# Kernel optimization log

Hardware: AMD Instinct MI355X
Metric: run time of the kernel (lower is better)

## Reference

```python
import jax, jax.numpy as jnp
import numpy as np

B, S, D, F, E = 8, 2048, 768, 3072, 8


def setup_inputs() -> dict:
    key = jax.random.key(0)
    k1, k2, k3, k4 = jax.random.split(key, 4)
    return {
        "hidden_states": jax.random.normal(k1, (B, S, D), dtype=jnp.float32),
        "router_w": jax.random.normal(k2, (D, E), dtype=jnp.float32) * 0.02,
        "w_in": jax.random.normal(k3, (E, D, F), dtype=jnp.float32) * 0.02,
        "w_out": jax.random.normal(k4, (E, F, D), dtype=jnp.float32) * 0.02,
    }


def reference(hidden_states, router_w, w_in, w_out):
    b, s, d = hidden_states.shape
    x = hidden_states.reshape(-1, d)                    # [T, D] tokens
    router_logits = x @ router_w                        # [T, E]
    router_probs_full = jax.nn.softmax(router_logits, axis=-1)
    expert_index = jnp.argmax(router_probs_full, axis=-1)          # top-1 routing
    onehot = jax.nn.one_hot(expert_index, E, dtype=x.dtype)        # [T, E] router_mask
    top_prob = jnp.max(router_probs_full, axis=-1, keepdims=True)  # [T, 1] router_probs

    # Per-expert FFN (relu MLP); every token is processed by exactly one expert,
    # expert outputs overwrite the token (gather/scatter combine in the original).
    y = jnp.zeros_like(x)
    for e in range(E):  # fixed small expert count; weights structurally distinct
        h = jax.nn.relu(x @ w_in[e]) @ w_out[e]
        y = y + onehot[:, e:e + 1] * h

    out = (top_prob * y).reshape(b, s, d)
    return out, router_logits, expert_index
```

## Files before the change

kernel.cpp:

```cpp
#include <hip/hip_runtime.h>
#include <hip/hip_bf16.h>

constexpr int T  = 16384;
constexpr int Dh = 768;
constexpr int Fh = 3072;
constexpr int Eh = 8;
constexpr int MAXT2 = T / 256 + Eh;

typedef unsigned short ushort_t;
typedef __attribute__((ext_vector_type(8))) short  bf16x8;
typedef __attribute__((ext_vector_type(4))) float  f32x4;

static __device__ __forceinline__ ushort_t f2bf(float f) {
    unsigned u = __builtin_bit_cast(unsigned, f);
    u += 0x7FFFu + ((u >> 16) & 1u);
    return (ushort_t)(u >> 16);
}

__global__ __launch_bounds__(1024) void router_kernel(
    const float* __restrict__ x, const float* __restrict__ rw,
    float* __restrict__ logits_out, float* __restrict__ eidx_out,
    float* __restrict__ topp, int* __restrict__ counts, int* __restrict__ perm) {

    __shared__ float rwT[Eh][Dh];
    __shared__ int   sAmax[16];
    __shared__ int   sBase[Eh];

    int tid = threadIdx.x;
    for (int i = tid; i < Dh * Eh; i += 1024) {
        int d = i >> 3, e = i & 7;
        rwT[e][d] = rw[i];
    }
    __syncthreads();

    int wave = tid >> 6, lane = tid & 63;
    int t = blockIdx.x * 16 + wave;
    const float* xr = x + (size_t)t * Dh;

    double acc[Eh];
#pragma unroll
    for (int e = 0; e < Eh; ++e) acc[e] = 0.0;

#pragma unroll
    for (int j = 0; j < Dh / 256; ++j) {
        int d = lane * 4 + j * 256;
        const float4 xv = *(const float4*)(xr + d);
#pragma unroll
        for (int e = 0; e < Eh; ++e) {
            const float4 w = *(const float4*)&rwT[e][d];
            acc[e] += (double)xv.x * (double)w.x + (double)xv.y * (double)w.y
                    + (double)xv.z * (double)w.z + (double)xv.w * (double)w.w;
        }
    }
#pragma unroll
    for (int off = 32; off > 0; off >>= 1) {
#pragma unroll
        for (int e = 0; e < Eh; ++e) acc[e] += __shfl_xor(acc[e], off, 64);
    }

    int amax = 0;
    if (lane == 0) {
        float l32[Eh];
        float m = -3.4e38f;
#pragma unroll
        for (int e = 0; e < Eh; ++e) l32[e] = (float)acc[e];
#pragma unroll
        for (int e = 0; e < Eh; ++e) {
            if (l32[e] > m) { m = l32[e]; amax = e; }
        }
        float s = 0.f;
#pragma unroll
        for (int e = 0; e < Eh; ++e) s += expf(l32[e] - m);
#pragma unroll
        for (int e = 0; e < Eh; ++e) logits_out[(size_t)t * Eh + e] = l32[e];
        eidx_out[t] = (float)amax;
        topp[t]     = 1.0f / s;
        sAmax[wave] = amax;
    }
    __syncthreads();

    if (tid < Eh) {
        int c = 0;
#pragma unroll
        for (int w = 0; w < 16; ++w) c += (sAmax[w] == tid);
        sBase[tid] = (c > 0) ? atomicAdd(&counts[tid], c) : 0;
    }
    __syncthreads();

    if (lane == 0) {
        int prior = 0;
        for (int w = 0; w < wave; ++w) prior += (sAmax[w] == amax);
        perm[amax * T + sBase[amax] + prior] = t;
    }
}

__global__ void scan_counts(const int* counts, int* offsets,
                            int* tE, int* tGoff, int* tSlot0, int* tRows, int* nT) {
    int lane = threadIdx.x;
    if (lane < Eh) {
        int coff = 0, toff = 0;
        for (int e = 0; e < lane; ++e) {
            int ce = counts[e];
            coff += ce;
            toff += (ce + 255) >> 8;
        }
        int c = counts[lane];
        offsets[lane] = coff;
        int myt = (c + 255) >> 8;
        for (int k = 0; k < myt; ++k) {
            int idx = toff + k;
            tE[idx]     = lane;
            tGoff[idx]  = coff + k * 256;
            tSlot0[idx] = k * 256;
            int rem = c - k * 256;
            tRows[idx]  = rem < 256 ? rem : 256;
        }
        if (lane == Eh - 1) {
            offsets[Eh] = coff + c;
            nT[0] = toff + myt;
        }
    }
}

__global__ void gather_cast_x(const float* __restrict__ x, const int* __restrict__ offsets,
                              const int* __restrict__ perm, ushort_t* __restrict__ Xg) {
    __shared__ int soff[Eh + 1];
    if (threadIdx.x < Eh + 1) soff[threadIdx.x] = offsets[threadIdx.x];
    __syncthreads();
    int q  = blockIdx.x * 256 + threadIdx.x;
    int g  = q / (Dh / 4);
    int cq = (q - g * (Dh / 4)) * 4;
    int e = 0;
#pragma unroll
    for (int i = 1; i < Eh; ++i) e += (g >= soff[i]);
    int tok = perm[e * T + (g - soff[e])];
    const float4 v = *(const float4*)(x + (size_t)tok * Dh + cq);
    ushort4 o;
    o.x = f2bf(v.x); o.y = f2bf(v.y); o.z = f2bf(v.z); o.w = f2bf(v.w);
    *(ushort4*)(Xg + (size_t)g * Dh + cq) = o;
}

__global__ void transpose_cvt(const float* __restrict__ src, ushort_t* __restrict__ dst,
                              int R, int C) {
    __shared__ ushort_t tile[32][33];
    int tx = threadIdx.x, ty = threadIdx.y;
    size_t base = (size_t)blockIdx.z * (size_t)R * (size_t)C;
    int c0 = blockIdx.x * 32, r0 = blockIdx.y * 32;
#pragma unroll
    for (int j = 0; j < 4; ++j) {
        int r = ty + j * 8;
        tile[r][tx] = f2bf(src[base + (size_t)(r0 + r) * C + c0 + tx]);
    }
    __syncthreads();
    int idx = ty * 32 + tx;
#pragma unroll
    for (int j = 0; j < 2; ++j) {
        int lin = idx + j * 256;
        int c  = lin >> 4;
        int rp = (lin & 15) * 2;
        ushort2 o = { tile[rp][c], tile[rp + 1][c] };
        *(ushort2*)(dst + base + (size_t)(c0 + c) * R + r0 + rp) = o;
    }
}

template<int KTOT, int NTOT, int MODE>
__global__ __launch_bounds__(512, 2) void moe_gemm2(
    const ushort_t* __restrict__ Aall, const ushort_t* __restrict__ Ball,
    const int* __restrict__ tE, const int* __restrict__ tGoff,
    const int* __restrict__ tSlot0, const int* __restrict__ tRows,
    const int* __restrict__ nT,
    const int* __restrict__ perm, const float* __restrict__ topp,
    void* __restrict__ Cout)
{
    int i = blockIdx.x;
    if (i >= nT[0]) return;
    int e     = tE[i];
    int goff  = tGoff[i];
    int slot0 = tSlot0[i];
    int rows  = tRows[i];
    int n0    = blockIdx.y * 256;

    const ushort_t* Ap = Aall + (size_t)goff * KTOT;
    const ushort_t* Bp = Ball + (size_t)e * KTOT * NTOT + (size_t)n0 * KTOT;

    __shared__ ushort_t As[2][256 * 64];
    __shared__ ushort_t Bs[2][256 * 64];
    __shared__ int   tokLds[256];
    __shared__ float probLds[256];

    int tid = threadIdx.x, lane = tid & 63, wid = tid >> 6;
    int wr = wid >> 2, wc = wid & 3;
    int gq = lane >> 4, lm = lane & 15, l7 = lane & 7;

    if (MODE == 1 && tid < 256) {
        int tok = (tid < rows) ? perm[e * T + slot0 + tid] : 0;
        tokLds[tid]  = tok;
        probLds[tid] = (tid < rows) ? topp[tok] : 0.f;
    }

    f32x4 acc[8][4];
    const f32x4 zero = {0.f, 0.f, 0.f, 0.f};
#pragma unroll
    for (int mi = 0; mi < 8; ++mi)
#pragma unroll
        for (int ni = 0; ni < 4; ++ni) acc[mi][ni] = zero;

    bf16x8 af[2][2];
    bf16x8 bb[2][4];

#define STAGE_A(BUF, KT) { \
    _Pragma("unroll") \
    for (int j = 0; j < 4; ++j) { \
        int c_ = tid + j * 512; \
        int rr = c_ >> 3, gg = c_ & 7; \
        int srow_ = rr < rows ? rr : rows - 1; \
        const ushort_t* src_ = Ap + (size_t)srow_ * KTOT + (size_t)(KT) * 64 + ((gg ^ (rr & 7)) << 3); \
        __builtin_amdgcn_global_load_lds( \
            (const __attribute__((address_space(1))) unsigned int*)src_, \
            (__attribute__((address_space(3))) unsigned int*)&As[BUF][rr * 64 + gg * 8], 16, 0, 0); \
    } }

#define STAGE_B(BUF, KT) { \
    _Pragma("unroll") \
    for (int j = 0; j < 4; ++j) { \
        int c_ = tid + j * 512; \
        int rr = c_ >> 3, gg = c_ & 7; \
        const ushort_t* src_ = Bp + (size_t)rr * KTOT + (size_t)(KT) * 64 + ((gg ^ (rr & 7)) << 3); \
        __builtin_amdgcn_global_load_lds( \
            (const __attribute__((address_space(1))) unsigned int*)src_, \
            (__attribute__((address_space(3))) unsigned int*)&Bs[BUF][rr * 64 + gg * 8], 16, 0, 0); \
    } }

#define READ_A(TB, P) { \
    _Pragma("unroll") \
    for (int ks = 0; ks < 2; ++ks) \
        _Pragma("unroll") \
        for (int j = 0; j < 2; ++j) \
            af[ks][j] = *(const bf16x8*)&As[TB][ \
                (wr * 128 + ((P) * 2 + j) * 16 + lm) * 64 + ((((ks << 2) + gq) ^ l7) << 3)]; \
    }

#define READ_B(TB) { \
    _Pragma("unroll") \
    for (int ks = 0; ks < 2; ++ks) \
        _Pragma("unroll") \
        for (int ni = 0; ni < 4; ++ni) \
            bb[ks][ni] = *(const bf16x8*)&Bs[TB][ \
                (wc * 64 + ni * 16 + lm) * 64 + ((((ks << 2) + gq) ^ l7) << 3)]; \
    }

#define MFMA_P(P) { \
    __builtin_amdgcn_s_setprio(1); \
    _Pragma("unroll") \
    for (int ks = 0; ks < 2; ++ks) \
        _Pragma("unroll") \
        for (int j = 0; j < 2; ++j) \
            _Pragma("unroll") \
            for (int ni = 0; ni < 4; ++ni) \
                acc[(P) * 2 + j][ni] = __builtin_amdgcn_mfma_f32_16x16x32_bf16( \
                    af[ks][j], bb[ks][ni], acc[(P) * 2 + j][ni], 0, 0, 0); \
    __builtin_amdgcn_s_setprio(0); }

    const int nkt = KTOT / 64;

    STAGE_A(0, 0);
    STAGE_B(0, 0);
    if (nkt > 1) {
        STAGE_B(1, 1);
        asm volatile("s_waitcnt vmcnt(4)" ::: "memory");
    } else {
        asm volatile("s_waitcnt vmcnt(0)" ::: "memory");
    }
    __builtin_amdgcn_sched_barrier(0);
    __builtin_amdgcn_s_barrier();

    for (int t = 0; t < nkt; ++t) {
        const int TB = t & 1;

        READ_B(TB);
        READ_A(TB, 0);
        if (t + 1 < nkt) STAGE_A(TB ^ 1, t + 1);
        __builtin_amdgcn_s_barrier();
        MFMA_P(0);
        __builtin_amdgcn_s_barrier();

        READ_A(TB, 1);
        if (t + 2 < nkt) STAGE_B(TB, t + 2);
        __builtin_amdgcn_s_barrier();
        MFMA_P(1);
        __builtin_amdgcn_s_barrier();

        READ_A(TB, 2);
        __builtin_amdgcn_s_barrier();
        MFMA_P(2);
        __builtin_amdgcn_s_barrier();

        READ_A(TB, 3);
        if (t + 2 < nkt) {
            asm volatile("s_waitcnt vmcnt(4)" ::: "memory");
            __builtin_amdgcn_sched_barrier(0);
        } else if (t + 1 < nkt) {
            asm volatile("s_waitcnt vmcnt(0)" ::: "memory");
            __builtin_amdgcn_sched_barrier(0);
        }
        __builtin_amdgcn_s_barrier();
        MFMA_P(3);
        __builtin_amdgcn_s_barrier();
    }

    int cr = (lane >> 4) * 4;
    int cc = lane & 15;
#pragma unroll
    for (int mi = 0; mi < 8; ++mi) {
#pragma unroll
        for (int r = 0; r < 4; ++r) {
            int m = wr * 128 + mi * 16 + cr + r;
            if (m < rows) {
                if (MODE == 0) {
                    ushort_t* hp = (ushort_t*)Cout + (size_t)(goff + m) * NTOT
                                 + n0 + wc * 64 + cc;
#pragma unroll
                    for (int ni = 0; ni < 4; ++ni) {
                        float v = acc[mi][ni][r];
                        hp[ni * 16] = f2bf(v > 0.f ? v : 0.f);
                    }
                } else {
                    int tok = tokLds[m];
                    float p = probLds[m];
                    float* op = (float*)Cout + (size_t)tok * NTOT
                              + n0 + wc * 64 + cc;
#pragma unroll
                    for (int ni = 0; ni < 4; ++ni) op[ni * 16] = acc[mi][ni][r] * p;
                }
            }
        }
    }
#undef STAGE_A
#undef STAGE_B
#undef READ_A
#undef READ_B
#undef MFMA_P
}

constexpr size_t OFF_COUNTS  = 0;
constexpr size_t OFF_OFFSETS = 256;
constexpr size_t OFF_TILES   = 512;
constexpr size_t OFF_TOPP    = OFF_TILES + 4 * 144 * 5 + 64;
constexpr size_t OFF_PERM    = OFF_TOPP + (size_t)T * 4;
constexpr size_t OFF_XG      = (OFF_PERM + (size_t)Eh * T * 4 + 255) & ~(size_t)255;
constexpr size_t OFF_H       = (OFF_XG + (size_t)(T + 128) * Dh * 2 + 255) & ~(size_t)255;
constexpr size_t OFF_WIN     = (OFF_H + (size_t)(T + 128) * Fh * 2 + 255) & ~(size_t)255;
constexpr size_t OFF_WOUT    = (OFF_WIN + (size_t)Eh * Dh * Fh * 2 + 255) & ~(size_t)255;

extern "C" void kernel_launch(void* const* d_in, const int* in_sizes, int n_in,
                              void* d_out, int out_size, void* d_ws, size_t ws_size,
                              hipStream_t stream) {
    const float* x    = (const float*)d_in[0];
    const float* rw   = (const float*)d_in[1];
    const float* w_in = (const float*)d_in[2];
    const float* w_out= (const float*)d_in[3];

    float* out    = (float*)d_out;
    float* logits = out + (size_t)T * Dh;
    float* eidx   = logits + (size_t)T * Eh;

    char* ws = (char*)d_ws;
    int*      counts  = (int*)(ws + OFF_COUNTS);
    int*      offsets = (int*)(ws + OFF_OFFSETS);
    int*      tE      = (int*)(ws + OFF_TILES);
    int*      tGoff   = tE + 144;
    int*      tSlot0  = tGoff + 144;
    int*      tRows   = tSlot0 + 144;
    int*      nT      = tRows + 144;
    float*    topp    = (float*)(ws + OFF_TOPP);
    int*      perm    = (int*)(ws + OFF_PERM);
    ushort_t* Xg      = (ushort_t*)(ws + OFF_XG);
    ushort_t* h       = (ushort_t*)(ws + OFF_H);
    ushort_t* WinT    = (ushort_t*)(ws + OFF_WIN);
    ushort_t* WoutT   = (ushort_t*)(ws + OFF_WOUT);

    hipMemsetAsync(counts, 0, Eh * sizeof(int), stream);
    router_kernel<<<T / 16, 1024, 0, stream>>>(x, rw, logits, eidx, topp, counts, perm);
    scan_counts<<<1, 64, 0, stream>>>(counts, offsets, tE, tGoff, tSlot0, tRows, nT);
    gather_cast_x<<<(T * (Dh / 4)) / 256, 256, 0, stream>>>(x, offsets, perm, Xg);
    transpose_cvt<<<dim3(Fh / 32, Dh / 32, Eh), dim3(32, 8), 0, stream>>>(w_in, WinT, Dh, Fh);
    transpose_cvt<<<dim3(Dh / 32, Fh / 32, Eh), dim3(32, 8), 0, stream>>>(w_out, WoutT, Fh, Dh);
    moe_gemm2<Dh, Fh, 0><<<dim3(MAXT2, Fh / 256), 512, 0, stream>>>(
        Xg, WinT, tE, tGoff, tSlot0, tRows, nT, perm, topp, (void*)h);
    moe_gemm2<Fh, Dh, 1><<<dim3(MAXT2, Dh / 256), 512, 0, stream>>>(
        h, WoutT, tE, tGoff, tSlot0, tRows, nT, perm, topp, (void*)out);
}
```

Before: 518.1 us.

## Software-pipeline LDS fragment reads with MFMAs and cut per-tile barriers

Restructures the GEMM inner loop so that A fragments for the next 16-row slice are read from LDS while MFMAs for the current slice run, using double-buffered register fragments. The next k-tile's first A and B fragments are prefetched before the trailing barrier. Barriers per k-tile drop from eight to two. This is meant to hide LDS latency and reduce synchronization stalls, at the cost of more live registers and tighter ordering assumptions around the async global-to-LDS loads.

```diff
diff --git a/kernel.cpp b/kernel.cpp
--- a/kernel.cpp
+++ b/kernel.cpp
@@ -205,8 +205,8 @@
 #pragma unroll
         for (int ni = 0; ni < 4; ++ni) acc[mi][ni] = zero;
 
-    bf16x8 af[2][2];
-    bf16x8 bb[2][4];
+    bf16x8 bb0[4], bb1[4];
+    bf16x8 afb[2][2];
 
 #define STAGE_A(BUF, KT) { \
     _Pragma("unroll") \
@@ -231,34 +231,26 @@
             (__attribute__((address_space(3))) unsigned int*)&Bs[BUF][rr * 64 + gg * 8], 16, 0, 0); \
     } }
 
-#define READ_A(TB, P) { \
+#define READ_B_KS(TB_, KS, DST) { \
+    _Pragma("unroll") \
+    for (int ni = 0; ni < 4; ++ni) \
+        DST[ni] = *(const bf16x8*)&Bs[TB_][ \
+            (wc * 64 + ni * 16 + lm) * 64 + (((((KS) << 2) + gq) ^ l7) << 3)]; \
+    }
+
+#define READ_A_MI(TB_, MI, DST) { \
     _Pragma("unroll") \
     for (int ks = 0; ks < 2; ++ks) \
-        _Pragma("unroll") \
-        for (int j = 0; j < 2; ++j) \
-            af[ks][j] = *(const bf16x8*)&As[TB][ \
-                (wr * 128 + ((P) * 2 + j) * 16 + lm) * 64 + ((((ks << 2) + gq) ^ l7) << 3)]; \
-    }
-
-#define READ_B(TB) { \
-    _Pragma("unroll") \
-    for (int ks = 0; ks < 2; ++ks) \
-        _Pragma("unroll") \
-        for (int ni = 0; ni < 4; ++ni) \
-            bb[ks][ni] = *(const bf16x8*)&Bs[TB][ \
-                (wc * 64 + ni * 16 + lm) * 64 + ((((ks << 2) + gq) ^ l7) << 3)]; \
-    }
-
-#define MFMA_P(P) { \
+        DST[ks] = *(const bf16x8*)&As[TB_][ \
+            (wr * 128 + (MI) * 16 + lm) * 64 + ((((ks << 2) + gq) ^ l7) << 3)]; \
+    }
+
+#define MFMA_KS(MI, SRC, KS, BB) { \
     __builtin_amdgcn_s_setprio(1); \
     _Pragma("unroll") \
-    for (int ks = 0; ks < 2; ++ks) \
-        _Pragma("unroll") \
-        for (int j = 0; j < 2; ++j) \
-            _Pragma("unroll") \
-            for (int ni = 0; ni < 4; ++ni) \
-                acc[(P) * 2 + j][ni] = __builtin_amdgcn_mfma_f32_16x16x32_bf16( \
-                    af[ks][j], bb[ks][ni], acc[(P) * 2 + j][ni], 0, 0, 0); \
+    for (int ni = 0; ni < 4; ++ni) \
+        acc[MI][ni] = __builtin_amdgcn_mfma_f32_16x16x32_bf16( \
+            SRC[KS], BB[ni], acc[MI][ni], 0, 0, 0); \
     __builtin_amdgcn_s_setprio(0); }
 
     const int nkt = KTOT / 64;
@@ -273,38 +265,42 @@
     }
     __builtin_amdgcn_sched_barrier(0);
     __builtin_amdgcn_s_barrier();
+    READ_B_KS(0, 0, bb0);
+    READ_B_KS(0, 1, bb1);
+    READ_A_MI(0, 0, afb[0]);
 
     for (int t = 0; t < nkt; ++t) {
         const int TB = t & 1;
 
-        READ_B(TB);
-        READ_A(TB, 0);
         if (t + 1 < nkt) STAGE_A(TB ^ 1, t + 1);
+        asm volatile("s_waitcnt lgkmcnt(0)" ::: "memory");
+        __builtin_amdgcn_sched_barrier(0);
         __builtin_amdgcn_s_barrier();
-        MFMA_P(0);
-        __builtin_amdgcn_s_barrier();
-
-        READ_A(TB, 1);
         if (t + 2 < nkt) STAGE_B(TB, t + 2);
-        __builtin_amdgcn_s_barrier();
-        MFMA_P(1);
-        __builtin_amdgcn_s_barrier();
-
-        READ_A(TB, 2);
-        __builtin_amdgcn_s_barrier();
-        MFMA_P(2);
-        __builtin_amdgcn_s_barrier();
-
-        READ_A(TB, 3);
-        if (t + 2 < nkt) {
-            asm volatile("s_waitcnt vmcnt(4)" ::: "memory");
+
+#pragma unroll
+        for (int mi = 0; mi < 7; ++mi) {
+            READ_A_MI(TB, mi + 1, afb[(mi + 1) & 1]);
+            MFMA_KS(mi, afb[mi & 1], 0, bb0);
+            MFMA_KS(mi, afb[mi & 1], 1, bb1);
+        }
+
+        if (t + 1 < nkt) {
+            if (t + 2 < nkt) {
+                asm volatile("s_waitcnt vmcnt(4)" ::: "memory");
+            } else {
+                asm volatile("s_waitcnt vmcnt(0)" ::: "memory");
+            }
             __builtin_amdgcn_sched_barrier(0);
-        } else if (t + 1 < nkt) {
-            asm volatile("s_waitcnt vmcnt(0)" ::: "memory");
-            __builtin_amdgcn_sched_barrier(0);
-        }
-        __builtin_amdgcn_s_barrier();
-        MFMA_P(3);
+            READ_A_MI(TB ^ 1, 0, afb[0]);
+            MFMA_KS(7, afb[1], 0, bb0);
+            READ_B_KS(TB ^ 1, 0, bb0);
+            MFMA_KS(7, afb[1], 1, bb1);
+            READ_B_KS(TB ^ 1, 1, bb1);
+        } else {
+            MFMA_KS(7, afb[1], 0, bb0);
+            MFMA_KS(7, afb[1], 1, bb1);
+        }
         __builtin_amdgcn_s_barrier();
     }
 
@@ -337,9 +333,9 @@
     }
 #undef STAGE_A
 #undef STAGE_B
-#undef READ_A
-#undef READ_B
-#undef MFMA_P
+#undef READ_B_KS
+#undef READ_A_MI
+#undef MFMA_KS
 }
 
 constexpr size_t OFF_COUNTS  = 0;
```

New measurement: 499.8 us. 3.5% less time.
